# Kernel tuning notes

Measured on AMD Instinct MI355X. Metric: run time of the kernel, lower is better.

Reference implementation:

```python
import jax, jax.numpy as jnp
import numpy as np

B, S, D, H, DFF, K = 16, 1024, 1024, 16, 4096, 3


def setup_inputs() -> dict:
    key = jax.random.key(0)
    ks = jax.random.split(key, 8)
    f = lambda k, sh: jax.random.normal(k, sh, jnp.float32) * 0.02
    return dict(
        x=jax.random.normal(ks[0], (B, S, D), jnp.float32),
        mask=jnp.ones((B, 1, S), jnp.int32),
        alpha1=jnp.ones((D,), jnp.float32), bias1=jnp.zeros((D,), jnp.float32),
        alpha2=jnp.ones((D,), jnp.float32), bias2=jnp.zeros((D,), jnp.float32),
        W_l1=f(ks[1], (D, 2 * D)), b_l1=jnp.zeros((2 * D,), jnp.float32),
        conv_w=f(ks[2], (H, K)),
        W_l2=f(ks[3], (D, D)), b_l2=jnp.zeros((D,), jnp.float32),
        W_ff1=f(ks[4], (D, DFF)), b_ff1=jnp.zeros((DFF,), jnp.float32),
        W_ff2=f(ks[5], (DFF, D)), b_ff2=jnp.zeros((D,), jnp.float32),
    )


def _norm(x, alpha, bias, eps=1e-6):
    # Norm: alpha * (x - mean) / (std + eps) + bias, torch std is unbiased (ddof=1)
    mu = x.mean(-1, keepdims=True)
    sd = x.std(-1, keepdims=True, ddof=1)
    return alpha * (x - mu) / (sd + eps) + bias


def _lightconv(x, conv_w):
    # x: [B, S, C]; conv_w: [H, K] softmax-normalized over K; channels in a head share kernel
    C = x.shape[-1]
    w = jax.nn.softmax(conv_w, axis=-1)              # [H, K]
    wk = jnp.repeat(w, C // H, axis=0)[:, None, :]   # [C, 1, K] depthwise kernel
    y = jax.lax.conv_general_dilated(
        x.transpose(0, 2, 1), wk, (1,), [(K // 2, (K - 1) // 2)],
        dimension_numbers=('NCH', 'OIH', 'NCH'), feature_group_count=C)
    return y.transpose(0, 2, 1)


def reference(x, mask, alpha1, bias1, alpha2, bias2, W_l1, b_l1, conv_w,
              W_l2, b_l2, W_ff1, b_ff1, W_ff2, b_ff2):
    # --- lightweight-conv sublayer ---
    res = x
    h = _norm(x, alpha1, bias1)
    h = h @ W_l1 + b_l1                         # [B,S,2C]
    a, b = jnp.split(h, 2, axis=-1)
    h = a * jax.nn.sigmoid(b)                   # GLU -> [B,S,C]
    cm = mask[:, -1, :][:, :, None]             # [B,S,1]
    h = jnp.where(cm == 0, 0.0, h)
    h = _lightconv(h, conv_w)
    h = h @ W_l2 + b_l2
    x = res + h
    # --- FFN sublayer ---
    res = x
    h = _norm(x, alpha2, bias2)
    h = jax.nn.relu(h @ W_ff1 + b_ff1) @ W_ff2 + b_ff2
    return res + h
```

## Files before the change

kernel.cpp:

```cpp
#include <hip/hip_runtime.h>

typedef unsigned short ushort_t;
typedef __attribute__((ext_vector_type(8))) short s8v;
typedef __attribute__((ext_vector_type(4))) float f4v;

__device__ __forceinline__ float b2f(ushort_t h) {
    union { unsigned u; float f; } c; c.u = ((unsigned)h) << 16; return c.f;
}
__device__ __forceinline__ ushort_t f2b(float f) {
    union { float f; unsigned u; } c; c.f = f;
    unsigned u = c.u;
    return (ushort_t)((u + 0x7fffu + ((u >> 16) & 1u)) >> 16);
}

__device__ __forceinline__ void glds16(const void* g, void* l) {
    __builtin_amdgcn_global_load_lds(
        (const __attribute__((address_space(1))) void*)g,
        (__attribute__((address_space(3))) void*)l, 16, 0, 0);
}

template <int PERM>
__global__ __launch_bounds__(256) void trans_k(const float* __restrict__ W,
                                               ushort_t* __restrict__ Wt,
                                               int K, int N) {
    __shared__ float tile[64][65];
    int k0 = blockIdx.x * 64, n0 = blockIdx.y * 64;
    int t = threadIdx.x;
    int c = t & 63, r4 = t >> 6;
#pragma unroll
    for (int i = 0; i < 16; ++i) {
        int r = i * 4 + r4;
        tile[r][c] = W[(size_t)(k0 + r) * N + n0 + c];
    }
    __syncthreads();
#pragma unroll
    for (int i = 0; i < 16; ++i) {
        int r = i * 4 + r4;
        int s = n0 + r;
        int d;
        if (PERM) {
            int a = (s < 1024);
            int s2 = a ? s : s - 1024;
            d = ((s2 >> 7) << 8) + (a ? 0 : 128) + (s2 & 127);
        } else {
            d = s;
        }
        Wt[(size_t)d * K + k0 + c] = f2b(tile[c][r]);
    }
}

__global__ __launch_bounds__(256) void norm_k(const float* __restrict__ x,
                                              const float* __restrict__ al,
                                              const float* __restrict__ be,
                                              ushort_t* __restrict__ out) {
    int row = blockIdx.x;
    const float4* xr = (const float4*)(x + (size_t)row * 1024);
    float4 v = xr[threadIdx.x];
    float s = v.x + v.y + v.z + v.w;
    float q = v.x * v.x + v.y * v.y + v.z * v.z + v.w * v.w;
#pragma unroll
    for (int o = 32; o > 0; o >>= 1) {
        s += __shfl_down(s, o);
        q += __shfl_down(q, o);
    }
    __shared__ float ss[4], qq[4];
    int lane = threadIdx.x & 63, wv = threadIdx.x >> 6;
    if (lane == 0) { ss[wv] = s; qq[wv] = q; }
    __syncthreads();
    s = ss[0] + ss[1] + ss[2] + ss[3];
    q = qq[0] + qq[1] + qq[2] + qq[3];
    float mu = s * (1.f / 1024.f);
    float var = (q - 1024.f * mu * mu) * (1.f / 1023.f);
    var = fmaxf(var, 0.f);
    float inv = 1.f / (sqrtf(var) + 1e-6f);
    float4 a4 = ((const float4*)al)[threadIdx.x];
    float4 b4 = ((const float4*)be)[threadIdx.x];
    ushort4 o4;
    o4.x = f2b(a4.x * (v.x - mu) * inv + b4.x);
    o4.y = f2b(a4.y * (v.y - mu) * inv + b4.y);
    o4.z = f2b(a4.z * (v.z - mu) * inv + b4.z);
    o4.w = f2b(a4.w * (v.w - mu) * inv + b4.w);
    ((ushort4*)(out + (size_t)row * 1024))[threadIdx.x] = o4;
}

__global__ __launch_bounds__(256) void conv_k(const ushort_t* __restrict__ g,
                                              const float* __restrict__ cw,
                                              ushort_t* __restrict__ out) {
    int i = blockIdx.x * 256 + threadIdx.x;
    int row = i >> 7;
    int cc = (i & 127) << 3;
    int s = row & 1023;
    int head = cc >> 6;
    float w0 = cw[head * 3 + 0], w1 = cw[head * 3 + 1], w2 = cw[head * 3 + 2];
    float mx = fmaxf(w0, fmaxf(w1, w2));
    float e0 = __expf(w0 - mx), e1 = __expf(w1 - mx), e2 = __expf(w2 - mx);
    float inv = 1.f / (e0 + e1 + e2);
    w0 = e0 * inv; w1 = e1 * inv; w2 = e2 * inv;
    size_t base = (size_t)row * 1024 + cc;
    s8v z = {0, 0, 0, 0, 0, 0, 0, 0};
    s8v vm = (s > 0)    ? *(const s8v*)(g + base - 1024) : z;
    s8v v0 = *(const s8v*)(g + base);
    s8v vp = (s < 1023) ? *(const s8v*)(g + base + 1024) : z;
    s8v ov;
#pragma unroll
    for (int j = 0; j < 8; ++j) {
        float r = w0 * b2f((ushort_t)vm[j]) + w1 * b2f((ushort_t)v0[j]) +
                  w2 * b2f((ushort_t)vp[j]);
        ov[j] = (short)f2b(r);
    }
    *(s8v*)(out + base) = ov;
}

template <int EPI>
__global__ __launch_bounds__(512, 1) void gemm_k(const ushort_t* __restrict__ A,
                                                 const ushort_t* __restrict__ Bt,
                                                 const float* __restrict__ bias,
                                                 const int* __restrict__ maskp,
                                                 const float* res, float* outf,
                                                 ushort_t* outb, int N, int K) {
    __shared__ char smem[131072] __attribute__((aligned(128)));
    const int NBN = N >> 8;
    const int per = gridDim.x >> 3;
    const int tt = (blockIdx.x & 7) * per + (blockIdx.x >> 3);
    const int gw = NBN << 3;
    const int g = tt / gw;
    const int rem = tt - g * gw;
    const int bm = (g << 3) + (rem & 7);
    const int bn = rem >> 3;

    const int t = threadIdx.x;
    const int l = t & 63, w = t >> 6;
    const int wm = w >> 2, wn = w & 3;
    const int lr = l & 15, lk = l >> 4;

    const int swzel = (((t & 3) ^ ((t >> 3) & 3)) << 3);
    const int r0 = t >> 2;
    const ushort_t* pA0 = A + (size_t)(bm * 256 + r0) * K + swzel;
    const ushort_t* pA1 = pA0 + (size_t)128 * K;
    const ushort_t* pB0 = Bt + (size_t)(bn * 256 + r0) * K + swzel;
    const ushort_t* pB1 = pB0 + (size_t)128 * K;

    const int fswz = ((lk ^ ((lr >> 1) & 3)) << 4);
    int aoff[8], boff[4];
#pragma unroll
    for (int m = 0; m < 8; ++m)
        aoff[m] = (wm * 128 + m * 16 + lr) * 64 + fswz;
#pragma unroll
    for (int n = 0; n < 4; ++n)
        boff[n] = 16384 + (wn * 64 + n * 16 + lr) * 64 + fswz;

    f4v acc[8][4];
#pragma unroll
    for (int m = 0; m < 8; ++m)
#pragma unroll
        for (int n = 0; n < 4; ++n) acc[m][n] = f4v{0.f, 0.f, 0.f, 0.f};

    const int NK = K >> 5;

#pragma unroll
    for (int p = 0; p < 3; ++p) {
        char* d = smem + p * 32768 + t * 16;
        glds16(pA0 + p * 32, d);
        glds16(pA1 + p * 32, d + 8192);
        glds16(pB0 + p * 32, d + 16384);
        glds16(pB1 + p * 32, d + 24576);
    }
    asm volatile("s_waitcnt vmcnt(8)");
    __builtin_amdgcn_s_barrier();
    __builtin_amdgcn_sched_barrier(0);

    s8v aL0[4], bF0[4], aL1[4], bF1[4], aH[4];
#pragma unroll
    for (int m = 0; m < 4; ++m) aL0[m] = *(const s8v*)(smem + aoff[m]);
#pragma unroll
    for (int n = 0; n < 4; ++n) bF0[n] = *(const s8v*)(smem + boff[n]);

#define KSTEP(I, CAL, CBF, NAL, NBF)                                           \
    {                                                                          \
        const int i_ = (I);                                                    \
        const char* cb_ = smem + (size_t)(i_ & 3) * 32768;                     \
        const char* nb_ = smem + (size_t)((i_ + 1) & 3) * 32768;               \
        int st_ = i_ + 3; if (st_ >= NK) st_ = NK - 1;                         \
        char* sd_ = smem + (size_t)((i_ + 3) & 3) * 32768 + t * 16;            \
        const int ko_ = st_ * 32;                                              \
        _Pragma("unroll")                                                      \
        for (int m = 0; m < 4; ++m) aH[m] = *(const s8v*)(cb_ + aoff[4 + m]);  \
        glds16(pA0 + ko_, sd_);                                                \
        glds16(pA1 + ko_, sd_ + 8192);                                         \
        glds16(pB0 + ko_, sd_ + 16384);                                        \
        glds16(pB1 + ko_, sd_ + 24576);                                        \
        __builtin_amdgcn_s_setprio(1);                                         \
        _Pragma("unroll")                                                      \
        for (int m = 0; m < 4; ++m)                                            \
            _Pragma("unroll")                                                  \
            for (int n = 0; n < 4; ++n)                                        \
                acc[m][n] = __builtin_amdgcn_mfma_f32_16x16x32_bf16(           \
                    CAL[m], CBF[n], acc[m][n], 0, 0, 0);                       \
        __builtin_amdgcn_s_setprio(0);                                         \
        __builtin_amdgcn_sched_barrier(0);                                     \
        asm volatile("s_waitcnt vmcnt(6)");                                    \
        __builtin_amdgcn_s_barrier();                                          \
        __builtin_amdgcn_sched_barrier(0);                                     \
        _Pragma("unroll")                                                      \
        for (int m = 0; m < 4; ++m) NAL[m] = *(const s8v*)(nb_ + aoff[m]);     \
        _Pragma("unroll")                                                      \
        for (int n = 0; n < 4; ++n) NBF[n] = *(const s8v*)(nb_ + boff[n]);     \
        __builtin_amdgcn_s_setprio(1);                                         \
        _Pragma("unroll")                                                      \
        for (int m = 0; m < 4; ++m)                                            \
            _Pragma("unroll")                                                  \
            for (int n = 0; n < 4; ++n)                                        \
                acc[4 + m][n] = __builtin_amdgcn_mfma_f32_16x16x32_bf16(       \
                    aH[m], CBF[n], acc[4 + m][n], 0, 0, 0);                    \
        __builtin_amdgcn_s_setprio(0);                                         \
    }

    for (int ii = 0; ii < NK; ii += 2) {
        KSTEP(ii, aL0, bF0, aL1, bF1);
        KSTEP(ii + 1, aL1, bF1, aL0, bF0);
    }
#undef KSTEP

    if (EPI == 1) {
#pragma unroll
        for (int n = 0; n < 4; ++n) {
            int gcol = bn * 256 + wn * 64 + n * 16 + lr;
            float bb = bias[gcol];
#pragma unroll
            for (int m = 0; m < 8; ++m) {
#pragma unroll
                for (int r = 0; r < 4; ++r) {
                    int grow = bm * 256 + wm * 128 + m * 16 + lk * 4 + r;
                    size_t oi = (size_t)grow * N + gcol;
                    outf[oi] = acc[m][n][r] + bb + res[oi];
                }
            }
        }
    } else {
        asm volatile("s_waitcnt vmcnt(0)" ::: "memory");
        __builtin_amdgcn_s_barrier();
        float bb4[4];
#pragma unroll
        for (int n = 0; n < 4; ++n) {
            int d = bn * 256 + wn * 64 + n * 16 + lr;
            int src = ((d >> 8) << 7) + (d & 127) + (((d >> 7) & 1) << 10);
            bb4[n] = bias[src];
        }
#pragma unroll
        for (int m = 0; m < 8; ++m)
#pragma unroll
            for (int n = 0; n < 4; ++n)
#pragma unroll
                for (int r = 0; r < 4; ++r) {
                    int row = wm * 128 + m * 16 + lk * 4 + r;
                    int colb = ((wn * 64 + n * 16 + lr) * 2) ^ ((row & 3) << 4);
                    *(ushort_t*)(smem + row * 512 + colb) =
                        f2b(acc[m][n][r] + bb4[n]);
                }
        __builtin_amdgcn_s_barrier();
#pragma unroll
        for (int s = 0; s < 8; ++s) {
            int row = s * 32 + (t >> 4);
            int abyt = row * 512 + (((t & 15) * 16) ^ ((row & 3) << 4));
            s8v av = *(const s8v*)(smem + abyt);
            s8v bv = *(const s8v*)(smem + abyt + 256);
            int grow = bm * 256 + row;
            float mval = (maskp[grow] == 0) ? 0.f : 1.f;
            s8v ov;
#pragma unroll
            for (int j = 0; j < 8; ++j) {
                float a = b2f((ushort_t)av[j]);
                float xx = b2f((ushort_t)bv[j]);
                ov[j] = (short)f2b(a * mval / (1.f + __expf(-xx)));
            }
            *(s8v*)(outb + (size_t)grow * (N >> 1) + bn * 128 + (t & 15) * 8) =
                ov;
        }
    }
}

template <int EPI>
__global__ __launch_bounds__(512, 1) void gemm8p_k(
    const ushort_t* __restrict__ A, const ushort_t* __restrict__ Bt,
    const float* __restrict__ bias, const float* res, float* outf,
    ushort_t* outb, int N, int K) {
    __shared__ char smem[131072] __attribute__((aligned(128)));
    const int NBN = N >> 8;
    const int per = gridDim.x >> 3;
    const int tt = (blockIdx.x & 7) * per + (blockIdx.x >> 3);
    const int gw = NBN << 3;
    const int g = tt / gw;
    const int rem = tt - g * gw;
    const int bm = (g << 3) + (rem & 7);
    const int bn = rem >> 3;

    const int t = threadIdx.x;
    const int l = t & 63, w = t >> 6;
    const int wm = w >> 2, wn = w & 3;
    const int lr = l & 15, lk = l >> 4;
    const int t16 = t * 16;

    const int srcsl = (((t & 7) ^ ((t >> 3) & 7)) << 3);
    const int rs = t >> 3;
    const ushort_t* pAL0 = A + (size_t)(bm * 256 + rs) * K + srcsl;
    const ushort_t* pAL1 = pAL0 + (size_t)64 * K;
    const ushort_t* pAH0 = pAL0 + (size_t)128 * K;
    const ushort_t* pAH1 = pAL0 + (size_t)192 * K;
    const ushort_t* pBL0 = Bt + (size_t)(bn * 256 + rs) * K + srcsl;
    const ushort_t* pBL1 = pBL0 + (size_t)64 * K;
    const ushort_t* pBH0 = pBL0 + (size_t)128 * K;
    const ushort_t* pBH1 = pBL0 + (size_t)192 * K;

    const int rowA = (wm * 16 + lr) * 128;
    const int rowB = (wn * 16 + lr) * 128;
    int xk[2];
#pragma unroll
    for (int ks = 0; ks < 2; ++ks)
        xk[ks] = (((ks * 4 + lk) ^ (lr & 7)) << 4);

    f4v acc[8][4];
#pragma unroll
    for (int m = 0; m < 8; ++m)
#pragma unroll
        for (int n = 0; n < 4; ++n) acc[m][n] = f4v{0.f, 0.f, 0.f, 0.f};

    const int NT = K >> 6;

#pragma unroll
    for (int p = 0; p < 2; ++p) {
        char* b = smem + p * 65536 + t16;
        const int ko = p * 64;
        glds16(pAL0 + ko, b);
        glds16(pAL1 + ko, b + 8192);
        glds16(pBL0 + ko, b + 32768);
        glds16(pBL1 + ko, b + 40960);
        glds16(pBH0 + ko, b + 49152);
        glds16(pBH1 + ko, b + 57344);
        glds16(pAH0 + ko, b + 16384);
        glds16(pAH1 + ko, b + 24576);
    }
    asm volatile("s_waitcnt vmcnt(8)");
    __builtin_amdgcn_s_barrier();

    s8v aR[4][2], bR[4][2];

#define MFMAQ(MB, NB)                                                          \
    _Pragma("unroll")                                                          \
    for (int ks = 0; ks < 2; ++ks)                                             \
        _Pragma("unroll")                                                      \
        for (int m = 0; m < 4; ++m)                                            \
            _Pragma("unroll")                                                  \
            for (int n = 0; n < 2; ++n)                                        \
                acc[(MB) + m][(NB) + n] =                                      \
                    __builtin_amdgcn_mfma_f32_16x16x32_bf16(                   \
                        aR[m][ks], bR[(NB) + n][ks],                           \
                        acc[(MB) + m][(NB) + n], 0, 0, 0);

#define KT(TI)                                                                 \
    {                                                                          \
        const int ti_ = (TI);                                                  \
        const char* cb_ = smem + (size_t)(ti_ & 1) * 65536;                    \
        char* sb_ = smem + (size_t)(ti_ & 1) * 65536;                          \
        int st_ = ti_ + 2;                                                     \
        if (st_ >= NT) st_ = NT - 2 + (ti_ & 1);                               \
        const int ko_ = st_ * 64;                                              \
                                                             \
        _Pragma("unroll")                                                      \
        for (int m = 0; m < 4; ++m)                                            \
            _Pragma("unroll")                                                  \
            for (int ks = 0; ks < 2; ++ks)                                     \
                aR[m][ks] = *(const s8v*)(cb_ + m * 4096 + rowA + xk[ks]);     \
        _Pragma("unroll")                                                      \
        for (int n = 0; n < 2; ++n)                                            \
            _Pragma("unroll")                                                  \
            for (int ks = 0; ks < 2; ++ks)                                     \
                bR[n][ks] =                                                    \
                    *(const s8v*)(cb_ + 32768 + n * 8192 + rowB + xk[ks]);     \
        asm volatile("s_waitcnt lgkmcnt(8)");                                  \
        __builtin_amdgcn_s_barrier();                                          \
        asm volatile("s_waitcnt lgkmcnt(0)");                                  \
        __builtin_amdgcn_s_setprio(1);                                         \
        MFMAQ(0, 0)                                                            \
        __builtin_amdgcn_s_setprio(0);                                         \
        __builtin_amdgcn_s_barrier();                                          \
                                                             \
        _Pragma("unroll")                                                      \
        for (int n = 0; n < 2; ++n)                                            \
            _Pragma("unroll")                                                  \
            for (int ks = 0; ks < 2; ++ks)                                     \
                bR[2 + n][ks] =                                                \
                    *(const s8v*)(cb_ + 49152 + n * 8192 + rowB + xk[ks]);     \
        glds16(pAL0 + ko_, sb_ + t16);                                         \
        glds16(pAL1 + ko_, sb_ + 8192 + t16);                                  \
        __builtin_amdgcn_s_barrier();                                          \
        asm volatile("s_waitcnt lgkmcnt(0)");                                  \
        __builtin_amdgcn_s_setprio(1);                                         \
        MFMAQ(0, 2)                                                            \
        __builtin_amdgcn_s_setprio(0);                                         \
        __builtin_amdgcn_s_barrier();                                          \
                                                             \
        _Pragma("unroll")                                                      \
        for (int m = 0; m < 4; ++m)                                            \
            _Pragma("unroll")                                                  \
            for (int ks = 0; ks < 2; ++ks)                                     \
                aR[m][ks] =                                                    \
                    *(const s8v*)(cb_ + 16384 + m * 4096 + rowA + xk[ks]);     \
        glds16(pBL0 + ko_, sb_ + 32768 + t16);                                 \
        glds16(pBL1 + ko_, sb_ + 40960 + t16);                                 \
        __builtin_amdgcn_s_barrier();                                          \
        asm volatile("s_waitcnt lgkmcnt(0)");                                  \
        __builtin_amdgcn_s_setprio(1);                                         \
        MFMAQ(4, 0)                                                            \
        __builtin_amdgcn_s_setprio(0);                                         \
        __builtin_amdgcn_s_barrier();                                          \
                                                             \
        glds16(pBH0 + ko_, sb_ + 49152 + t16);                                 \
        glds16(pBH1 + ko_, sb_ + 57344 + t16);                                 \
        glds16(pAH0 + ko_, sb_ + 16384 + t16);                                 \
        glds16(pAH1 + ko_, sb_ + 24576 + t16);                                 \
        asm volatile("s_waitcnt vmcnt(6)");                                    \
        __builtin_amdgcn_s_barrier();                                          \
        __builtin_amdgcn_s_setprio(1);                                         \
        MFMAQ(4, 2)                                                            \
        __builtin_amdgcn_s_setprio(0);                                         \
        __builtin_amdgcn_s_barrier();                                          \
    }

    for (int j = 0; j < NT; j += 2) {
        KT(j);
        KT(j + 1);
    }
#undef KT
#undef MFMAQ

    if (EPI == 1) {
#pragma unroll
        for (int n = 0; n < 4; ++n) {
            int gcol = bn * 256 + n * 64 + wn * 16 + lr;
            float bb = bias[gcol];
#pragma unroll
            for (int m = 0; m < 8; ++m) {
#pragma unroll
                for (int r = 0; r < 4; ++r) {
                    int grow = bm * 256 + m * 32 + wm * 16 + lk * 4 + r;
                    size_t oi = (size_t)grow * N + gcol;
                    outf[oi] = acc[m][n][r] + bb + res[oi];
                }
            }
        }
    } else {
        asm volatile("s_waitcnt vmcnt(0)" ::: "memory");
        __builtin_amdgcn_s_barrier();
        float bb4[4];
#pragma unroll
        for (int n = 0; n < 4; ++n)
            bb4[n] = bias[bn * 256 + n * 64 + wn * 16 + lr];
#pragma unroll
        for (int m = 0; m < 8; ++m)
#pragma unroll
            for (int n = 0; n < 4; ++n)
#pragma unroll
                for (int r = 0; r < 4; ++r) {
                    int row = m * 32 + wm * 16 + lk * 4 + r;
                    int colb =
                        ((n * 64 + wn * 16 + lr) * 2) ^ ((row & 3) << 4);
                    *(ushort_t*)(smem + row * 512 + colb) =
                        f2b(fmaxf(acc[m][n][r] + bb4[n], 0.f));
                }
        __builtin_amdgcn_s_barrier();
#pragma unroll
        for (int s = 0; s < 16; ++s) {
            int row = s * 16 + (t >> 5);
            int byt = row * 512 + (((t & 31) * 16) ^ ((row & 3) << 4));
            int grow = bm * 256 + row;
            int gcol = bn * 256 + (t & 31) * 8;
            *(s8v*)(outb + (size_t)grow * N + gcol) = *(const s8v*)(smem + byt);
        }
    }
}

extern "C" void kernel_launch(void* const* d_in, const int* in_sizes, int n_in,
                              void* d_out, int out_size, void* d_ws, size_t ws_size,
                              hipStream_t stream) {
    const float* x      = (const float*)d_in[0];
    const int*   mask   = (const int*)d_in[1];
    const float* alpha1 = (const float*)d_in[2];
    const float* bias1  = (const float*)d_in[3];
    const float* alpha2 = (const float*)d_in[4];
    const float* bias2  = (const float*)d_in[5];
    const float* W_l1   = (const float*)d_in[6];
    const float* b_l1   = (const float*)d_in[7];
    const float* conv_w = (const float*)d_in[8];
    const float* W_l2   = (const float*)d_in[9];
    const float* b_l2   = (const float*)d_in[10];
    const float* W_ff1  = (const float*)d_in[11];
    const float* b_ff1  = (const float*)d_in[12];
    const float* W_ff2  = (const float*)d_in[13];
    const float* b_ff2  = (const float*)d_in[14];
    float* out = (float*)d_out;

    char* ws = (char*)d_ws;
    size_t off = 0;
    auto alloc = [&](size_t b) {
        char* p = ws + off;
        off += (b + 255) & ~(size_t)255;
        return p;
    };
    ushort_t* Wl1t  = (ushort_t*)alloc(2048ull * 1024 * 2);
    ushort_t* Wl2t  = (ushort_t*)alloc(1024ull * 1024 * 2);
    ushort_t* Wff1t = (ushort_t*)alloc(4096ull * 1024 * 2);
    ushort_t* Wff2t = (ushort_t*)alloc(1024ull * 4096 * 2);
    char* regA = alloc(134217728ull);
    ushort_t* B1 = (ushort_t*)alloc(33554432ull);
    ushort_t* C1 = (ushort_t*)alloc(33554432ull);
    ushort_t* G1 = (ushort_t*)regA;
    ushort_t* f1 = (ushort_t*)regA;

    const int R = 16384;

    trans_k<1><<<dim3(16, 32), 256, 0, stream>>>(W_l1, Wl1t, 1024, 2048);
    trans_k<0><<<dim3(16, 16), 256, 0, stream>>>(W_l2, Wl2t, 1024, 1024);
    trans_k<0><<<dim3(16, 64), 256, 0, stream>>>(W_ff1, Wff1t, 1024, 4096);
    trans_k<0><<<dim3(64, 16), 256, 0, stream>>>(W_ff2, Wff2t, 4096, 1024);

    norm_k<<<R, 256, 0, stream>>>(x, alpha1, bias1, B1);
    gemm_k<3><<<64 * 8, 512, 0, stream>>>(B1, Wl1t, b_l1, mask, nullptr,
                                          nullptr, G1, 2048, 1024);
    conv_k<<<8192, 256, 0, stream>>>(G1, conv_w, C1);
    gemm8p_k<1><<<64 * 4, 512, 0, stream>>>(C1, Wl2t, b_l2, x, out, nullptr,
                                            1024, 1024);

    norm_k<<<R, 256, 0, stream>>>(out, alpha2, bias2, B1);
    gemm8p_k<2><<<64 * 16, 512, 0, stream>>>(B1, Wff1t, b_ff1, nullptr,
                                             nullptr, f1, 4096, 1024);
    gemm8p_k<1><<<64 * 4, 512, 0, stream>>>(f1, Wff2t, b_ff2, out, out,
                                            nullptr, 1024, 4096);
}
```

Baseline: 510.5 us.

## Halve GEMM LDS to double buffering so two blocks fit per CU

The generic GEMM kernel drops from a four-stage 128 KB LDS ring to a two-stage 64 KB double buffer. It waits for all outstanding loads before each barrier and writes the epilogue in two halves through the reduced LDS. Because each block now needs half the shared memory, two blocks can share a CU and hide each other's latency. The FFN1 GEMM moves from the gemm8p kernel to this one. The cost is a shallower prefetch (vmcnt(0) at every step), which exposes more global-load latency within each block.

```diff
diff --git a/kernel.cpp b/kernel.cpp
--- a/kernel.cpp
+++ b/kernel.cpp
@@ -112,13 +112,11 @@
 }
 
 template <int EPI>
-__global__ __launch_bounds__(512, 1) void gemm_k(const ushort_t* __restrict__ A,
-                                                 const ushort_t* __restrict__ Bt,
-                                                 const float* __restrict__ bias,
-                                                 const int* __restrict__ maskp,
-                                                 const float* res, float* outf,
-                                                 ushort_t* outb, int N, int K) {
-    __shared__ char smem[131072] __attribute__((aligned(128)));
+__global__ __launch_bounds__(512, 1) void gemm2r_k(
+    const ushort_t* __restrict__ A, const ushort_t* __restrict__ Bt,
+    const float* __restrict__ bias, const int* __restrict__ maskp,
+    ushort_t* outb, int N, int K) {
+    __shared__ char smem[65536] __attribute__((aligned(128)));
     const int NBN = N >> 8;
     const int per = gridDim.x >> 3;
     const int tt = (blockIdx.x & 7) * per + (blockIdx.x >> 3);
@@ -157,15 +155,11 @@
 
     const int NK = K >> 5;
 
-#pragma unroll
-    for (int p = 0; p < 3; ++p) {
-        char* d = smem + p * 32768 + t * 16;
-        glds16(pA0 + p * 32, d);
-        glds16(pA1 + p * 32, d + 8192);
-        glds16(pB0 + p * 32, d + 16384);
-        glds16(pB1 + p * 32, d + 24576);
-    }
-    asm volatile("s_waitcnt vmcnt(8)");
+    glds16(pA0, smem + t * 16);
+    glds16(pA1, smem + 8192 + t * 16);
+    glds16(pB0, smem + 16384 + t * 16);
+    glds16(pB1, smem + 24576 + t * 16);
+    asm volatile("s_waitcnt vmcnt(0)");
     __builtin_amdgcn_s_barrier();
     __builtin_amdgcn_sched_barrier(0);
 
@@ -175,14 +169,15 @@
 #pragma unroll
     for (int n = 0; n < 4; ++n) bF0[n] = *(const s8v*)(smem + boff[n]);
 
-#define KSTEP(I, CAL, CBF, NAL, NBF)                                           \
+#define KSTEP2(I, CAL, CBF, NAL, NBF)                                          \
     {                                                                          \
         const int i_ = (I);                                                    \
-        const char* cb_ = smem + (size_t)(i_ & 3) * 32768;                     \
-        const char* nb_ = smem + (size_t)((i_ + 1) & 3) * 32768;               \
-        int st_ = i_ + 3; if (st_ >= NK) st_ = NK - 1;                         \
-        char* sd_ = smem + (size_t)((i_ + 3) & 3) * 32768 + t * 16;            \
+        const char* cb_ = smem + (size_t)(i_ & 1) * 32768;                     \
+        const char* nb_ = smem + (size_t)((i_ + 1) & 1) * 32768;               \
+        int st_ = i_ + 1; if (st_ >= NK) st_ = NK - 1;                         \
+        char* sd_ = smem + (size_t)((i_ + 1) & 1) * 32768 + t * 16;            \
         const int ko_ = st_ * 32;                                              \
+                               \
         _Pragma("unroll")                                                      \
         for (int m = 0; m < 4; ++m) aH[m] = *(const s8v*)(cb_ + aoff[4 + m]);  \
         glds16(pA0 + ko_, sd_);                                                \
@@ -198,9 +193,10 @@
                     CAL[m], CBF[n], acc[m][n], 0, 0, 0);                       \
         __builtin_amdgcn_s_setprio(0);                                         \
         __builtin_amdgcn_sched_barrier(0);                                     \
-        asm volatile("s_waitcnt vmcnt(6)");                                    \
+        asm volatile("s_waitcnt vmcnt(0)");               \
         __builtin_amdgcn_s_barrier();                                          \
         __builtin_amdgcn_sched_barrier(0);                                     \
+                                  \
         _Pragma("unroll")                                                      \
         for (int m = 0; m < 4; ++m) NAL[m] = *(const s8v*)(nb_ + aoff[m]);     \
         _Pragma("unroll")                                                      \
@@ -216,66 +212,67 @@
     }
 
     for (int ii = 0; ii < NK; ii += 2) {
-        KSTEP(ii, aL0, bF0, aL1, bF1);
-        KSTEP(ii + 1, aL1, bF1, aL0, bF0);
-    }
-#undef KSTEP
-
-    if (EPI == 1) {
-#pragma unroll
-        for (int n = 0; n < 4; ++n) {
-            int gcol = bn * 256 + wn * 64 + n * 16 + lr;
-            float bb = bias[gcol];
-#pragma unroll
-            for (int m = 0; m < 8; ++m) {
+        KSTEP2(ii, aL0, bF0, aL1, bF1);
+        KSTEP2(ii + 1, aL1, bF1, aL0, bF0);
+    }
+#undef KSTEP2
+
+    __builtin_amdgcn_s_barrier();
+    float bb4[4];
+#pragma unroll
+    for (int n = 0; n < 4; ++n) {
+        int d = bn * 256 + wn * 64 + n * 16 + lr;
+        int src = d;
+        if (EPI == 3)
+            src = ((d >> 8) << 7) + (d & 127) + (((d >> 7) & 1) << 10);
+        bb4[n] = bias[src];
+    }
+#pragma unroll
+    for (int h = 0; h < 2; ++h) {
+#pragma unroll
+        for (int m4 = 0; m4 < 4; ++m4)
+#pragma unroll
+            for (int n = 0; n < 4; ++n)
 #pragma unroll
                 for (int r = 0; r < 4; ++r) {
-                    int grow = bm * 256 + wm * 128 + m * 16 + lk * 4 + r;
-                    size_t oi = (size_t)grow * N + gcol;
-                    outf[oi] = acc[m][n][r] + bb + res[oi];
+                    int row = wm * 64 + m4 * 16 + lk * 4 + r;
+                    int colb = ((wn * 64 + n * 16 + lr) * 2) ^ ((row & 3) << 4);
+                    float v = acc[h * 4 + m4][n][r] + bb4[n];
+                    if (EPI == 2) v = fmaxf(v, 0.f);
+                    *(ushort_t*)(smem + row * 512 + colb) = f2b(v);
                 }
+        __builtin_amdgcn_s_barrier();
+        if (EPI == 3) {
+#pragma unroll
+            for (int s = 0; s < 4; ++s) {
+                int row = s * 32 + (t >> 4);
+                int abyt = row * 512 + (((t & 15) * 16) ^ ((row & 3) << 4));
+                s8v av = *(const s8v*)(smem + abyt);
+                s8v bv = *(const s8v*)(smem + abyt + 256);
+                int grow = bm * 256 + ((row >> 6) << 7) + 64 * h + (row & 63);
+                float mval = (maskp[grow] == 0) ? 0.f : 1.f;
+                s8v ov;
+#pragma unroll
+                for (int j = 0; j < 8; ++j) {
+                    float a = b2f((ushort_t)av[j]);
+                    float xx = b2f((ushort_t)bv[j]);
+                    ov[j] = (short)f2b(a * mval / (1.f + __expf(-xx)));
+                }
+                *(s8v*)(outb + (size_t)grow * (N >> 1) + bn * 128 +
+                        (t & 15) * 8) = ov;
+            }
+        } else {
+#pragma unroll
+            for (int s = 0; s < 8; ++s) {
+                int row = s * 16 + (t >> 5);
+                int byt = row * 512 + (((t & 31) * 16) ^ ((row & 3) << 4));
+                int grow = bm * 256 + ((row >> 6) << 7) + 64 * h + (row & 63);
+                int gcol = bn * 256 + (t & 31) * 8;
+                *(s8v*)(outb + (size_t)grow * N + gcol) =
+                    *(const s8v*)(smem + byt);
             }
         }
-    } else {
-        asm volatile("s_waitcnt vmcnt(0)" ::: "memory");
         __builtin_amdgcn_s_barrier();
-        float bb4[4];
-#pragma unroll
-        for (int n = 0; n < 4; ++n) {
-            int d = bn * 256 + wn * 64 + n * 16 + lr;
-            int src = ((d >> 8) << 7) + (d & 127) + (((d >> 7) & 1) << 10);
-            bb4[n] = bias[src];
-        }
-#pragma unroll
-        for (int m = 0; m < 8; ++m)
-#pragma unroll
-            for (int n = 0; n < 4; ++n)
-#pragma unroll
-                for (int r = 0; r < 4; ++r) {
-                    int row = wm * 128 + m * 16 + lk * 4 + r;
-                    int colb = ((wn * 64 + n * 16 + lr) * 2) ^ ((row & 3) << 4);
-                    *(ushort_t*)(smem + row * 512 + colb) =
-                        f2b(acc[m][n][r] + bb4[n]);
-                }
-        __builtin_amdgcn_s_barrier();
-#pragma unroll
-        for (int s = 0; s < 8; ++s) {
-            int row = s * 32 + (t >> 4);
-            int abyt = row * 512 + (((t & 15) * 16) ^ ((row & 3) << 4));
-            s8v av = *(const s8v*)(smem + abyt);
-            s8v bv = *(const s8v*)(smem + abyt + 256);
-            int grow = bm * 256 + row;
-            float mval = (maskp[grow] == 0) ? 0.f : 1.f;
-            s8v ov;
-#pragma unroll
-            for (int j = 0; j < 8; ++j) {
-                float a = b2f((ushort_t)av[j]);
-                float xx = b2f((ushort_t)bv[j]);
-                ov[j] = (short)f2b(a * mval / (1.f + __expf(-xx)));
-            }
-            *(s8v*)(outb + (size_t)grow * (N >> 1) + bn * 128 + (t & 15) * 8) =
-                ov;
-        }
     }
 }
 
@@ -524,15 +521,15 @@
     trans_k<0><<<dim3(64, 16), 256, 0, stream>>>(W_ff2, Wff2t, 4096, 1024);
 
     norm_k<<<R, 256, 0, stream>>>(x, alpha1, bias1, B1);
-    gemm_k<3><<<64 * 8, 512, 0, stream>>>(B1, Wl1t, b_l1, mask, nullptr,
-                                          nullptr, G1, 2048, 1024);
+    gemm2r_k<3><<<64 * 8, 512, 0, stream>>>(B1, Wl1t, b_l1, mask, G1, 2048,
+                                            1024);
     conv_k<<<8192, 256, 0, stream>>>(G1, conv_w, C1);
     gemm8p_k<1><<<64 * 4, 512, 0, stream>>>(C1, Wl2t, b_l2, x, out, nullptr,
                                             1024, 1024);
 
     norm_k<<<R, 256, 0, stream>>>(out, alpha2, bias2, B1);
-    gemm8p_k<2><<<64 * 16, 512, 0, stream>>>(B1, Wff1t, b_ff1, nullptr,
-                                             nullptr, f1, 4096, 1024);
+    gemm2r_k<2><<<64 * 16, 512, 0, stream>>>(B1, Wff1t, b_ff1, nullptr, f1,
+                                             4096, 1024);
     gemm8p_k<1><<<64 * 4, 512, 0, stream>>>(f1, Wff2t, b_ff2, out, out,
                                             nullptr, 1024, 4096);
 }
```

After: 539.0 us. 5.6% more time.

## Double-buffer register fragments in 8-phase GEMM to overlap LDS reads with MFMA

Applied to the files above, without the earlier changes.

Restructures the main loop of the 8-phase GEMM kernel used for the FFN and second conv GEMMs. It now keeps two sets of A/B register fragments, so LDS reads for the next quadrant (and next k-tile) are issued while the current MFMA quadrant runs. It also reorders the global-to-LDS prefetches and uses sched_barrier to pin instruction order. Separately, gemm_k's epilogue drops its EPI==1 branch and always runs the GLU path, which is only valid because gemm_k is called with EPI 3. The extra fragments raise register pressure, and the reordered waits and barriers risk LDS hazards or spills.

```diff
diff --git a/kernel.cpp b/kernel.cpp
--- a/kernel.cpp
+++ b/kernel.cpp
@@ -221,66 +221,48 @@
     }
 #undef KSTEP
 
-    if (EPI == 1) {
-#pragma unroll
-        for (int n = 0; n < 4; ++n) {
-            int gcol = bn * 256 + wn * 64 + n * 16 + lr;
-            float bb = bias[gcol];
-#pragma unroll
-            for (int m = 0; m < 8; ++m) {
-#pragma unroll
-                for (int r = 0; r < 4; ++r) {
-                    int grow = bm * 256 + wm * 128 + m * 16 + lk * 4 + r;
-                    size_t oi = (size_t)grow * N + gcol;
-                    outf[oi] = acc[m][n][r] + bb + res[oi];
-                }
+    asm volatile("s_waitcnt vmcnt(0)" ::: "memory");
+    __builtin_amdgcn_s_barrier();
+    float bb4[4];
+#pragma unroll
+    for (int n = 0; n < 4; ++n) {
+        int d = bn * 256 + wn * 64 + n * 16 + lr;
+        int src = ((d >> 8) << 7) + (d & 127) + (((d >> 7) & 1) << 10);
+        bb4[n] = bias[src];
+    }
+#pragma unroll
+    for (int m = 0; m < 8; ++m)
+#pragma unroll
+        for (int n = 0; n < 4; ++n)
+#pragma unroll
+            for (int r = 0; r < 4; ++r) {
+                int row = wm * 128 + m * 16 + lk * 4 + r;
+                int colb = ((wn * 64 + n * 16 + lr) * 2) ^ ((row & 3) << 4);
+                *(ushort_t*)(smem + row * 512 + colb) =
+                    f2b(acc[m][n][r] + bb4[n]);
             }
+    __builtin_amdgcn_s_barrier();
+#pragma unroll
+    for (int s = 0; s < 8; ++s) {
+        int row = s * 32 + (t >> 4);
+        int abyt = row * 512 + (((t & 15) * 16) ^ ((row & 3) << 4));
+        s8v av = *(const s8v*)(smem + abyt);
+        s8v bv = *(const s8v*)(smem + abyt + 256);
+        int grow = bm * 256 + row;
+        float mval = (maskp[grow] == 0) ? 0.f : 1.f;
+        s8v ov;
+#pragma unroll
+        for (int j = 0; j < 8; ++j) {
+            float a = b2f((ushort_t)av[j]);
+            float xx = b2f((ushort_t)bv[j]);
+            ov[j] = (short)f2b(a * mval / (1.f + __expf(-xx)));
         }
-    } else {
-        asm volatile("s_waitcnt vmcnt(0)" ::: "memory");
-        __builtin_amdgcn_s_barrier();
-        float bb4[4];
-#pragma unroll
-        for (int n = 0; n < 4; ++n) {
-            int d = bn * 256 + wn * 64 + n * 16 + lr;
-            int src = ((d >> 8) << 7) + (d & 127) + (((d >> 7) & 1) << 10);
-            bb4[n] = bias[src];
-        }
-#pragma unroll
-        for (int m = 0; m < 8; ++m)
-#pragma unroll
-            for (int n = 0; n < 4; ++n)
-#pragma unroll
-                for (int r = 0; r < 4; ++r) {
-                    int row = wm * 128 + m * 16 + lk * 4 + r;
-                    int colb = ((wn * 64 + n * 16 + lr) * 2) ^ ((row & 3) << 4);
-                    *(ushort_t*)(smem + row * 512 + colb) =
-                        f2b(acc[m][n][r] + bb4[n]);
-                }
-        __builtin_amdgcn_s_barrier();
-#pragma unroll
-        for (int s = 0; s < 8; ++s) {
-            int row = s * 32 + (t >> 4);
-            int abyt = row * 512 + (((t & 15) * 16) ^ ((row & 3) << 4));
-            s8v av = *(const s8v*)(smem + abyt);
-            s8v bv = *(const s8v*)(smem + abyt + 256);
-            int grow = bm * 256 + row;
-            float mval = (maskp[grow] == 0) ? 0.f : 1.f;
-            s8v ov;
-#pragma unroll
-            for (int j = 0; j < 8; ++j) {
-                float a = b2f((ushort_t)av[j]);
-                float xx = b2f((ushort_t)bv[j]);
-                ov[j] = (short)f2b(a * mval / (1.f + __expf(-xx)));
-            }
-            *(s8v*)(outb + (size_t)grow * (N >> 1) + bn * 128 + (t & 15) * 8) =
-                ov;
-        }
+        *(s8v*)(outb + (size_t)grow * (N >> 1) + bn * 128 + (t & 15) * 8) = ov;
     }
 }
 
 template <int EPI>
-__global__ __launch_bounds__(512, 1) void gemm8p_k(
+__global__ __launch_bounds__(512, 1) void gemmsp_k(
     const ushort_t* __restrict__ A, const ushort_t* __restrict__ Bt,
     const float* __restrict__ bias, const float* res, float* outf,
     ushort_t* outb, int N, int K) {
@@ -339,12 +321,23 @@
         glds16(pAH0 + ko, b + 16384);
         glds16(pAH1 + ko, b + 24576);
     }
-    asm volatile("s_waitcnt vmcnt(8)");
+    asm volatile("s_waitcnt vmcnt(8)" ::: "memory");
     __builtin_amdgcn_s_barrier();
-
-    s8v aR[4][2], bR[4][2];
-
-#define MFMAQ(MB, NB)                                                          \
+    __builtin_amdgcn_sched_barrier(0);
+
+    s8v A0[4][2], A1[4][2], B0[2][2], B1[2][2];
+#pragma unroll
+    for (int m = 0; m < 4; ++m)
+#pragma unroll
+        for (int ks = 0; ks < 2; ++ks)
+            A0[m][ks] = *(const s8v*)(smem + m * 4096 + rowA + xk[ks]);
+#pragma unroll
+    for (int n = 0; n < 2; ++n)
+#pragma unroll
+        for (int ks = 0; ks < 2; ++ks)
+            B0[n][ks] = *(const s8v*)(smem + 32768 + n * 8192 + rowB + xk[ks]);
+
+#define MFMAQ(AR, BR, MB, NB)                                                  \
     _Pragma("unroll")                                                          \
     for (int ks = 0; ks < 2; ++ks)                                             \
         _Pragma("unroll")                                                      \
@@ -353,84 +346,76 @@
             for (int n = 0; n < 2; ++n)                                        \
                 acc[(MB) + m][(NB) + n] =                                      \
                     __builtin_amdgcn_mfma_f32_16x16x32_bf16(                   \
-                        aR[m][ks], bR[(NB) + n][ks],                           \
-                        acc[(MB) + m][(NB) + n], 0, 0, 0);
-
-#define KT(TI)                                                                 \
-    {                                                                          \
-        const int ti_ = (TI);                                                  \
-        const char* cb_ = smem + (size_t)(ti_ & 1) * 65536;                    \
-        char* sb_ = smem + (size_t)(ti_ & 1) * 65536;                          \
-        int st_ = ti_ + 2;                                                     \
-        if (st_ >= NT) st_ = NT - 2 + (ti_ & 1);                               \
-        const int ko_ = st_ * 64;                                              \
-                                                             \
-        _Pragma("unroll")                                                      \
-        for (int m = 0; m < 4; ++m)                                            \
-            _Pragma("unroll")                                                  \
-            for (int ks = 0; ks < 2; ++ks)                                     \
-                aR[m][ks] = *(const s8v*)(cb_ + m * 4096 + rowA + xk[ks]);     \
-        _Pragma("unroll")                                                      \
-        for (int n = 0; n < 2; ++n)                                            \
-            _Pragma("unroll")                                                  \
-            for (int ks = 0; ks < 2; ++ks)                                     \
-                bR[n][ks] =                                                    \
-                    *(const s8v*)(cb_ + 32768 + n * 8192 + rowB + xk[ks]);     \
-        asm volatile("s_waitcnt lgkmcnt(8)");                                  \
-        __builtin_amdgcn_s_barrier();                                          \
-        asm volatile("s_waitcnt lgkmcnt(0)");                                  \
-        __builtin_amdgcn_s_setprio(1);                                         \
-        MFMAQ(0, 0)                                                            \
-        __builtin_amdgcn_s_setprio(0);                                         \
-        __builtin_amdgcn_s_barrier();                                          \
-                                                             \
-        _Pragma("unroll")                                                      \
-        for (int n = 0; n < 2; ++n)                                            \
-            _Pragma("unroll")                                                  \
-            for (int ks = 0; ks < 2; ++ks)                                     \
-                bR[2 + n][ks] =                                                \
-                    *(const s8v*)(cb_ + 49152 + n * 8192 + rowB + xk[ks]);     \
-        glds16(pAL0 + ko_, sb_ + t16);                                         \
-        glds16(pAL1 + ko_, sb_ + 8192 + t16);                                  \
-        __builtin_amdgcn_s_barrier();                                          \
-        asm volatile("s_waitcnt lgkmcnt(0)");                                  \
-        __builtin_amdgcn_s_setprio(1);                                         \
-        MFMAQ(0, 2)                                                            \
-        __builtin_amdgcn_s_setprio(0);                                         \
-        __builtin_amdgcn_s_barrier();                                          \
-                                                             \
-        _Pragma("unroll")                                                      \
-        for (int m = 0; m < 4; ++m)                                            \
-            _Pragma("unroll")                                                  \
-            for (int ks = 0; ks < 2; ++ks)                                     \
-                aR[m][ks] =                                                    \
-                    *(const s8v*)(cb_ + 16384 + m * 4096 + rowA + xk[ks]);     \
-        glds16(pBL0 + ko_, sb_ + 32768 + t16);                                 \
-        glds16(pBL1 + ko_, sb_ + 40960 + t16);                                 \
-        __builtin_amdgcn_s_barrier();                                          \
-        asm volatile("s_waitcnt lgkmcnt(0)");                                  \
-        __builtin_amdgcn_s_setprio(1);                                         \
-        MFMAQ(4, 0)                                                            \
-        __builtin_amdgcn_s_setprio(0);                                         \
-        __builtin_amdgcn_s_barrier();                                          \
-                                                             \
-        glds16(pBH0 + ko_, sb_ + 49152 + t16);                                 \
-        glds16(pBH1 + ko_, sb_ + 57344 + t16);                                 \
-        glds16(pAH0 + ko_, sb_ + 16384 + t16);                                 \
-        glds16(pAH1 + ko_, sb_ + 24576 + t16);                                 \
-        asm volatile("s_waitcnt vmcnt(6)");                                    \
-        __builtin_amdgcn_s_barrier();                                          \
-        __builtin_amdgcn_s_setprio(1);                                         \
-        MFMAQ(4, 2)                                                            \
-        __builtin_amdgcn_s_setprio(0);                                         \
-        __builtin_amdgcn_s_barrier();                                          \
-    }
-
-    for (int j = 0; j < NT; j += 2) {
-        KT(j);
-        KT(j + 1);
-    }
-#undef KT
+                        AR[m][ks], BR[n][ks], acc[(MB) + m][(NB) + n], 0, 0, 0);
+
+    for (int ti = 0; ti < NT; ++ti) {
+        const char* cb = smem + (size_t)(ti & 1) * 65536;
+        char* sb = smem + (size_t)(ti & 1) * 65536;
+        int st = ti + 2;
+        if (st >= NT) st = NT - 2 + (ti & 1);
+        const int ko = st * 64;
+        const int nti = (ti + 1 < NT) ? ti + 1 : NT - 1;
+        const char* nb = smem + (size_t)(nti & 1) * 65536;
+
+        asm volatile("s_waitcnt lgkmcnt(0)" ::: "memory");
+        __builtin_amdgcn_sched_barrier(0);
+        __builtin_amdgcn_s_setprio(1);
+        MFMAQ(A0, B0, 0, 0)
+        __builtin_amdgcn_s_setprio(0);
+#pragma unroll
+        for (int n = 0; n < 2; ++n)
+#pragma unroll
+            for (int ks = 0; ks < 2; ++ks)
+                B1[n][ks] =
+                    *(const s8v*)(cb + 49152 + n * 8192 + rowB + xk[ks]);
+        glds16(pAL0 + ko, sb + t16);
+        glds16(pAL1 + ko, sb + 8192 + t16);
+        glds16(pBL0 + ko, sb + 32768 + t16);
+        glds16(pBL1 + ko, sb + 40960 + t16);
+        __builtin_amdgcn_s_barrier();
+
+        asm volatile("s_waitcnt lgkmcnt(0)" ::: "memory");
+        __builtin_amdgcn_sched_barrier(0);
+        __builtin_amdgcn_s_setprio(1);
+        MFMAQ(A0, B1, 0, 2)
+        __builtin_amdgcn_s_setprio(0);
+#pragma unroll
+        for (int m = 0; m < 4; ++m)
+#pragma unroll
+            for (int ks = 0; ks < 2; ++ks)
+                A1[m][ks] =
+                    *(const s8v*)(cb + 16384 + m * 4096 + rowA + xk[ks]);
+        glds16(pBH0 + ko, sb + 49152 + t16);
+        glds16(pBH1 + ko, sb + 57344 + t16);
+        __builtin_amdgcn_s_barrier();
+
+        asm volatile("s_waitcnt lgkmcnt(0)" ::: "memory");
+        __builtin_amdgcn_sched_barrier(0);
+        __builtin_amdgcn_s_setprio(1);
+        MFMAQ(A1, B0, 4, 0)
+        __builtin_amdgcn_s_setprio(0);
+        glds16(pAH0 + ko, sb + 16384 + t16);
+        glds16(pAH1 + ko, sb + 24576 + t16);
+        __builtin_amdgcn_s_barrier();
+
+        __builtin_amdgcn_s_setprio(1);
+        MFMAQ(A1, B1, 4, 2)
+        __builtin_amdgcn_s_setprio(0);
+        asm volatile("s_waitcnt vmcnt(8)" ::: "memory");
+        __builtin_amdgcn_sched_barrier(0);
+#pragma unroll
+        for (int m = 0; m < 4; ++m)
+#pragma unroll
+            for (int ks = 0; ks < 2; ++ks)
+                A0[m][ks] = *(const s8v*)(nb + m * 4096 + rowA + xk[ks]);
+#pragma unroll
+        for (int n = 0; n < 2; ++n)
+#pragma unroll
+            for (int ks = 0; ks < 2; ++ks)
+                B0[n][ks] =
+                    *(const s8v*)(nb + 32768 + n * 8192 + rowB + xk[ks]);
+        __builtin_amdgcn_s_barrier();
+    }
 #undef MFMAQ
 
     if (EPI == 1) {
@@ -527,12 +512,12 @@
     gemm_k<3><<<64 * 8, 512, 0, stream>>>(B1, Wl1t, b_l1, mask, nullptr,
                                           nullptr, G1, 2048, 1024);
     conv_k<<<8192, 256, 0, stream>>>(G1, conv_w, C1);
-    gemm8p_k<1><<<64 * 4, 512, 0, stream>>>(C1, Wl2t, b_l2, x, out, nullptr,
+    gemmsp_k<1><<<64 * 4, 512, 0, stream>>>(C1, Wl2t, b_l2, x, out, nullptr,
                                             1024, 1024);
 
     norm_k<<<R, 256, 0, stream>>>(out, alpha2, bias2, B1);
-    gemm8p_k<2><<<64 * 16, 512, 0, stream>>>(B1, Wff1t, b_ff1, nullptr,
+    gemmsp_k<2><<<64 * 16, 512, 0, stream>>>(B1, Wff1t, b_ff1, nullptr,
                                              nullptr, f1, 4096, 1024);
-    gemm8p_k<1><<<64 * 4, 512, 0, stream>>>(f1, Wff2t, b_ff2, out, out,
+    gemmsp_k<1><<<64 * 4, 512, 0, stream>>>(f1, Wff2t, b_ff2, out, out,
                                             nullptr, 1024, 4096);
 }
```

Result: no change. 504.2 us (-1.2%).
